# Performance work log

Measured on AMD Instinct MI355X. Metric: run time of the kernel, lower is better.

## Reference

```python
import jax, jax.numpy as jnp
import numpy as np

R = 4  # box radius (init kwarg r)


def setup_inputs() -> dict:
    key = jax.random.key(0)
    x = jax.random.normal(key, (8, 16, 512, 512), dtype=jnp.float32)
    return {"x": x}


def reference(x) -> jnp.ndarray:
    r = R
    # Integral image: pad (r+1 before, r after) on H and W, then double cumsum.
    summed = jnp.pad(x, ((0, 0), (0, 0), (r + 1, r), (r + 1, r)))
    summed = jnp.cumsum(jnp.cumsum(summed, axis=2), axis=3)
    k = 2 * r + 1
    intersection = summed[:, :, :-k, :-k]
    union = summed[:, :, k:, k:]
    left = summed[:, :, :-k, k:]
    right = summed[:, :, k:, :-k]
    return union - left - right + intersection
```

## Files before the change

### kernel.cpp

```cpp
#include <hip/hip_runtime.h>


#define W   512
#define RR  16
#define NSTRIP (W / RR)

__device__ __forceinline__ float4 ld4(const float* p) { return *(const float4*)p; }
__device__ __forceinline__ float4 add4(float4 a, float4 b) {
    return make_float4(a.x + b.x, a.y + b.y, a.z + b.z, a.w + b.w);
}
__device__ __forceinline__ float4 sub4(float4 a, float4 b) {
    return make_float4(a.x - b.x, a.y - b.y, a.z - b.z, a.w - b.w);
}

__device__ __forceinline__ float lane_shr1(float x) {
    return __int_as_float(__builtin_amdgcn_update_dpp(
        0, __float_as_int(x), 0x138 , 0xF, 0xF, true));
}
__device__ __forceinline__ float lane_shl1(float x) {
    return __int_as_float(__builtin_amdgcn_update_dpp(
        0, __float_as_int(x), 0x130 , 0xF, 0xF, true));
}
__device__ __forceinline__ float4 lane_shr1_4(float4 v) {
    return make_float4(lane_shr1(v.x), lane_shr1(v.y), lane_shr1(v.z), lane_shr1(v.w));
}
__device__ __forceinline__ float4 lane_shl1_4(float4 v) {
    return make_float4(lane_shl1(v.x), lane_shl1(v.y), lane_shl1(v.z), lane_shl1(v.w));
}

__global__ __launch_bounds__(256, 2) void boxfilter9(const float* __restrict__ in,
                                                     float* __restrict__ out) {
    const int t     = threadIdx.x;
    const int l     = t & 63;
    const int wid   = t >> 6;
    const int unit  = blockIdx.x * 4 + wid;
    const int img   = unit >> 5;
    const int strip = unit & (NSTRIP - 1);

    const float* __restrict__ inp  = in  + (size_t)img * W * W;
    float* __restrict__       outp = out + (size_t)img * W * W;
    const int y0 = strip * RR;
    const int c0 = l << 3;

    auto compute_h = [&](int y, float4& h0, float4& h1) {
        if ((unsigned)y < W) {
            const float* row = inp + y * W + c0;
            float4 lo = ld4(row);
            float4 hi = ld4(row + 4);
            float4 ap = lane_shr1_4(hi);
            float4 an = lane_shl1_4(lo);
            float sa = (ap.x + ap.y) + (ap.z + ap.w);
            float sl = (lo.x + lo.y) + (lo.z + lo.w);
            h0.x = (sa + sl) + hi.x;
            h0.y = h0.x - ap.x + hi.y;
            h0.z = h0.y - ap.y + hi.z;
            h0.w = h0.z - ap.z + hi.w;
            h1.x = h0.w - ap.w + an.x;
            h1.y = h1.x - lo.x + an.y;
            h1.z = h1.y - lo.y + an.z;
            h1.w = h1.z - lo.z + an.w;
        } else {
            h0 = make_float4(0, 0, 0, 0);
            h1 = make_float4(0, 0, 0, 0);
        }
    };

    float4 ring0[9], ring1[9];
    float4 vs0 = make_float4(0, 0, 0, 0), vs1 = make_float4(0, 0, 0, 0);
    #pragma unroll
    for (int k = 0; k < 8; ++k) {
        compute_h(y0 - 4 + k, ring0[k], ring1[k]);
        vs0 = add4(vs0, ring0[k]);
        vs1 = add4(vs1, ring1[k]);
    }

    #pragma unroll
    for (int i = 0; i < RR; ++i) {
        float4 hn0, hn1;
        compute_h(y0 + 4 + i, hn0, hn1);
        float4 o0 = add4(vs0, hn0);
        float4 o1 = add4(vs1, hn1);
        float* orow = outp + (size_t)(y0 + i) * W + c0;
        *(float4*)(orow)     = o0;
        *(float4*)(orow + 4) = o1;
        vs0 = sub4(o0, ring0[i % 9]);
        vs1 = sub4(o1, ring1[i % 9]);
        ring0[(i + 8) % 9] = hn0;
        ring1[(i + 8) % 9] = hn1;
    }
}

extern "C" void kernel_launch(void* const* d_in, const int* in_sizes, int n_in,
                              void* d_out, int out_size, void* d_ws, size_t ws_size,
                              hipStream_t stream) {
    const float* x = (const float*)d_in[0];
    float* y = (float*)d_out;
    dim3 grid(128 * NSTRIP / 4);
    dim3 block(256);
    boxfilter9<<<grid, block, 0, stream>>>(x, y);
}
```

Baseline: 254.8 us.

## Split each row into two coalesced halves, use branchless clamped loads and nontemporal stores

Each lane now owns two 4-wide column groups, one in each half of the row, instead of 8 contiguous columns, so every float4 access is contiguous across the wave. Neighbour values at the half boundary come from DPP shifts plus readlane broadcasts. Out-of-range rows are handled by clamping the row index and multiplying by a 0/1 mask, which removes the branch. Output goes through nontemporal stores, and the ring buffer shrinks to 8 entries with power-of-two indexing. The trade-off is extra readlane, select and multiply instructions per row.

```diff
diff --git a/kernel.cpp b/kernel.cpp
--- a/kernel.cpp
+++ b/kernel.cpp
@@ -5,12 +5,21 @@
 #define RR  16
 #define NSTRIP (W / RR)
 
+typedef float vfloat4 __attribute__((ext_vector_type(4)));
+
 __device__ __forceinline__ float4 ld4(const float* p) { return *(const float4*)p; }
 __device__ __forceinline__ float4 add4(float4 a, float4 b) {
     return make_float4(a.x + b.x, a.y + b.y, a.z + b.z, a.w + b.w);
 }
 __device__ __forceinline__ float4 sub4(float4 a, float4 b) {
     return make_float4(a.x - b.x, a.y - b.y, a.z - b.z, a.w - b.w);
+}
+__device__ __forceinline__ float4 mul4s(float4 a, float m) {
+    return make_float4(a.x * m, a.y * m, a.z * m, a.w * m);
+}
+__device__ __forceinline__ void st4_nt(float* p, float4 v) {
+    vfloat4 q = { v.x, v.y, v.z, v.w };
+    __builtin_nontemporal_store(q, (vfloat4*)p);
 }
 
 __device__ __forceinline__ float lane_shr1(float x) {
@@ -27,6 +36,9 @@
 __device__ __forceinline__ float4 lane_shl1_4(float4 v) {
     return make_float4(lane_shl1(v.x), lane_shl1(v.y), lane_shl1(v.z), lane_shl1(v.w));
 }
+__device__ __forceinline__ float bcast(float x, int lane) {
+    return __int_as_float(__builtin_amdgcn_readlane(__float_as_int(x), lane));
+}
 
 __global__ __launch_bounds__(256, 2) void boxfilter9(const float* __restrict__ in,
                                                      float* __restrict__ out) {
@@ -40,53 +52,68 @@
     const float* __restrict__ inp  = in  + (size_t)img * W * W;
     float* __restrict__       outp = out + (size_t)img * W * W;
     const int y0 = strip * RR;
-    const int c0 = l << 3;
+    const int cA = l << 2;
+    const int cB = 256 + (l << 2);
 
-    auto compute_h = [&](int y, float4& h0, float4& h1) {
-        if ((unsigned)y < W) {
-            const float* row = inp + y * W + c0;
-            float4 lo = ld4(row);
-            float4 hi = ld4(row + 4);
-            float4 ap = lane_shr1_4(hi);
-            float4 an = lane_shl1_4(lo);
-            float sa = (ap.x + ap.y) + (ap.z + ap.w);
-            float sl = (lo.x + lo.y) + (lo.z + lo.w);
-            h0.x = (sa + sl) + hi.x;
-            h0.y = h0.x - ap.x + hi.y;
-            h0.z = h0.y - ap.y + hi.z;
-            h0.w = h0.z - ap.z + hi.w;
-            h1.x = h0.w - ap.w + an.x;
-            h1.y = h1.x - lo.x + an.y;
-            h1.z = h1.y - lo.y + an.z;
-            h1.w = h1.z - lo.z + an.w;
-        } else {
-            h0 = make_float4(0, 0, 0, 0);
-            h1 = make_float4(0, 0, 0, 0);
-        }
+    auto hchain = [](float4 p, float4 v, float4 n) -> float4 {
+        float sp = (p.x + p.y) + (p.z + p.w);
+        float sv = (v.x + v.y) + (v.z + v.w);
+        float4 h;
+        h.x = (sp + sv) + n.x;
+        h.y = h.x - p.x + n.y;
+        h.z = h.y - p.y + n.z;
+        h.w = h.z - p.z + n.w;
+        return h;
     };
 
-    float4 ring0[9], ring1[9];
-    float4 vs0 = make_float4(0, 0, 0, 0), vs1 = make_float4(0, 0, 0, 0);
+    auto compute_h = [&](int y, float4& hA, float4& hB) {
+        int yc = y < 0 ? 0 : (y > W - 1 ? W - 1 : y);
+        float m = (y == yc) ? 1.0f : 0.0f;
+        const float* row = inp + yc * W;
+        float4 vA = mul4s(ld4(row + cA), m);
+        float4 vB = mul4s(ld4(row + cB), m);
+        float4 pA = lane_shr1_4(vA);
+        float4 nA = lane_shl1_4(vA);
+        float4 pB = lane_shr1_4(vB);
+        float4 nB = lane_shl1_4(vB);
+        float a63x = bcast(vA.x, 63), a63y = bcast(vA.y, 63),
+              a63z = bcast(vA.z, 63), a63w = bcast(vA.w, 63);
+        float b0x  = bcast(vB.x, 0),  b0y  = bcast(vB.y, 0),
+              b0z  = bcast(vB.z, 0),  b0w  = bcast(vB.w, 0);
+        pB.x = (l == 0) ? a63x : pB.x;
+        pB.y = (l == 0) ? a63y : pB.y;
+        pB.z = (l == 0) ? a63z : pB.z;
+        pB.w = (l == 0) ? a63w : pB.w;
+        nA.x = (l == 63) ? b0x : nA.x;
+        nA.y = (l == 63) ? b0y : nA.y;
+        nA.z = (l == 63) ? b0z : nA.z;
+        nA.w = (l == 63) ? b0w : nA.w;
+        hA = hchain(pA, vA, nA);
+        hB = hchain(pB, vB, nB);
+    };
+
+    float4 ringA[8], ringB[8];
+    float4 vsA = make_float4(0, 0, 0, 0), vsB = make_float4(0, 0, 0, 0);
     #pragma unroll
     for (int k = 0; k < 8; ++k) {
-        compute_h(y0 - 4 + k, ring0[k], ring1[k]);
-        vs0 = add4(vs0, ring0[k]);
-        vs1 = add4(vs1, ring1[k]);
+        compute_h(y0 - 4 + k, ringA[k], ringB[k]);
+        vsA = add4(vsA, ringA[k]);
+        vsB = add4(vsB, ringB[k]);
     }
 
     #pragma unroll
     for (int i = 0; i < RR; ++i) {
-        float4 hn0, hn1;
-        compute_h(y0 + 4 + i, hn0, hn1);
-        float4 o0 = add4(vs0, hn0);
-        float4 o1 = add4(vs1, hn1);
-        float* orow = outp + (size_t)(y0 + i) * W + c0;
-        *(float4*)(orow)     = o0;
-        *(float4*)(orow + 4) = o1;
-        vs0 = sub4(o0, ring0[i % 9]);
-        vs1 = sub4(o1, ring1[i % 9]);
-        ring0[(i + 8) % 9] = hn0;
-        ring1[(i + 8) % 9] = hn1;
+        float4 hA, hB;
+        compute_h(y0 + 4 + i, hA, hB);
+        float4 oA = add4(vsA, hA);
+        float4 oB = add4(vsB, hB);
+        float* orow = outp + (size_t)(y0 + i) * W;
+        st4_nt(orow + cA, oA);
+        st4_nt(orow + cB, oB);
+        vsA = sub4(oA, ringA[i & 7]);
+        vsB = sub4(oB, ringB[i & 7]);
+        ringA[i & 7] = hA;
+        ringB[i & 7] = hB;
     }
 }
 
```

Measured after the change: 237.7 us. 6.7% less time.
